# Kernel optimization log

Hardware: AMD Instinct MI355X
Metric: run time of the kernel (lower is better)

The kernel has to match this reference:

```python
import jax, jax.numpy as jnp
import numpy as np

D_MODEL = 1024
NUM_HEADS = 16
D_K = 1024
D_V = 1024
D_IN = 1024
THETA = 10000.0
B, S = 2, 2048


def setup_inputs() -> dict:
    key = jax.random.key(0)
    k1, k2, k3, k4, k5 = jax.random.split(key, 5)
    std_qkv = (2.0 / (D_IN + D_K)) ** 0.5
    std_o = (2.0 / (D_V + D_MODEL)) ** 0.5
    x = jax.random.normal(k1, (B, S, D_IN), jnp.float32)
    wq = jax.random.normal(k2, (D_IN, D_K), jnp.float32) * std_qkv
    wk = jax.random.normal(k3, (D_IN, D_K), jnp.float32) * std_qkv
    wv = jax.random.normal(k4, (D_IN, D_V), jnp.float32) * std_qkv
    wo = jax.random.normal(k5, (D_V, D_MODEL), jnp.float32) * std_o
    return {"x": x, "wq": wq, "wk": wk, "wv": wv, "wo": wo}


def _rope(t, theta):
    # t: (H, B, S, hd) -- interleaved-pair RoPE, angles pos * theta^(-2i/hd)
    hd = t.shape[-1]
    inv_freq = 1.0 / (theta ** (jnp.arange(0, hd, 2, dtype=jnp.float32) / hd))  # (hd/2,)
    pos = jnp.arange(t.shape[-2], dtype=jnp.float32)
    ang = pos[:, None] * inv_freq[None, :]                                       # (S, hd/2)
    cos, sin = jnp.cos(ang), jnp.sin(ang)
    tp = t.reshape(t.shape[:-1] + (hd // 2, 2))
    t0, t1 = tp[..., 0], tp[..., 1]
    out = jnp.stack([t0 * cos - t1 * sin, t0 * sin + t1 * cos], axis=-1)
    return out.reshape(t.shape)


def reference(x, wq, wk, wv, wo):
    b, s, _ = x.shape
    hd = D_K // NUM_HEADS
    hdv = D_V // NUM_HEADS
    # fused QKV proj (math identical to concat-then-matmul)
    q = jnp.einsum('bsd,de->bse', x, wq).reshape(b, s, NUM_HEADS, hd).transpose(2, 0, 1, 3)
    k = jnp.einsum('bsd,de->bse', x, wk).reshape(b, s, NUM_HEADS, hd).transpose(2, 0, 1, 3)
    v = jnp.einsum('bsd,de->bse', x, wv).reshape(b, s, NUM_HEADS, hdv).transpose(2, 0, 1, 3)
    q = _rope(q, THETA)
    k = _rope(k, THETA)
    scale = 1.0 / jnp.sqrt(jnp.asarray(hd, jnp.float32))
    scores = jnp.einsum('hbqd,hbkd->hbqk', q, k) * scale                 # (H,B,S,S)
    causal = jnp.tril(jnp.ones((s, s), dtype=bool))
    scores = jnp.where(causal, scores, -jnp.inf)
    attn = jax.nn.softmax(scores, axis=-1)
    o = jnp.einsum('hbqk,hbkd->hbqd', attn, v)                            # (H,B,S,hdv)
    o = o.transpose(1, 2, 0, 3).reshape(b, s, D_V)                        # merge heads (outer)
    return jnp.einsum('bsd,de->bse', o, wo)
```

## Files before the change

kernel.cpp:

```cpp
#include <hip/hip_runtime.h>
#include <stdint.h>

typedef __attribute__((ext_vector_type(8))) short short8;
typedef __attribute__((ext_vector_type(4))) float f32x4;
typedef __attribute__((ext_vector_type(4))) unsigned short ushort4v;

static __device__ __forceinline__ unsigned short f2b(float f) {
  union { float f; unsigned int u; } v; v.f = f;
  unsigned int r = v.u + 0x7FFFu + ((v.u >> 16) & 1u);
  return (unsigned short)(r >> 16);
}

static __device__ __forceinline__ float exp2fast(float x) {
#if __has_builtin(__builtin_amdgcn_exp2f)
  return __builtin_amdgcn_exp2f(x);
#else
  return exp2f(x);
#endif
}

static __device__ __forceinline__ void gload16(const void* g, void* l) {
  __builtin_amdgcn_global_load_lds(
      (const __attribute__((address_space(1))) unsigned int*)g,
      (__attribute__((address_space(3))) unsigned int*)l, 16, 0, 0);
}


__global__ __launch_bounds__(256) void cast_x_kernel(const float* __restrict__ x,
                                                     unsigned short* __restrict__ xb) {
  int i = (blockIdx.x * 256 + threadIdx.x) * 4;
  float4 v = *(const float4*)(x + i);
  ushort4v o = { f2b(v.x), f2b(v.y), f2b(v.z), f2b(v.w) };
  *(ushort4v*)(xb + i) = o;
}

__global__ __launch_bounds__(256) void transpose_cast_kernel(
    const float* __restrict__ wq, const float* __restrict__ wk,
    const float* __restrict__ wv, const float* __restrict__ wo,
    unsigned short* __restrict__ wT) {
  const int z = blockIdx.z;
  const float* src = (z == 0) ? wq : (z == 1) ? wk : (z == 2) ? wv : wo;
  unsigned short* dst = wT + (size_t)z * 1048576;
  __shared__ float t[32][33];
  const int tid = threadIdx.x;
  const int tx = tid & 31, ty = tid >> 5;
  const int n0 = blockIdx.x * 32, k0 = blockIdx.y * 32;
#pragma unroll
  for (int i = 0; i < 4; ++i) {
    int r = ty + i * 8;
    t[r][tx] = src[(size_t)(k0 + r) * 1024 + n0 + tx];
  }
  __syncthreads();
#pragma unroll
  for (int i = 0; i < 4; ++i) {
    int r = ty + i * 8;
    dst[(size_t)(n0 + r) * 1024 + k0 + tx] = f2b(t[tx][r]);
  }
}

__global__ __launch_bounds__(256) void rope_tab_kernel(float* __restrict__ ct,
                                                       float* __restrict__ st) {
  int i = blockIdx.x * 256 + threadIdx.x;
  int s = i >> 5, p = i & 31;
  float ang = (float)s * powf(10000.0f, -(float)(2 * p) / 64.0f);
  ct[i] = cosf(ang);
  st[i] = sinf(ang);
}


__global__ __launch_bounds__(256) void gemm_kernel(
    const unsigned short* __restrict__ A, const unsigned short* __restrict__ WT,
    unsigned short* __restrict__ Qb, unsigned short* __restrict__ Kb,
    unsigned short* __restrict__ VTb, float* __restrict__ Fout,
    const float* __restrict__ ctab, const float* __restrict__ stab, int finalMode) {
  __shared__ unsigned short As[128 * 32];
  __shared__ unsigned short Bs[128 * 32];
  const int tid = threadIdx.x;
  const int w = tid >> 6, lane = tid & 63;
  const int m0 = blockIdx.x * 128, n0 = blockIdx.y * 128;
  int mode;
  const unsigned short* Bt;
  if (finalMode) { mode = 3; Bt = WT; }
  else { mode = blockIdx.z; Bt = WT + (size_t)mode * 1048576; }
  const int wr = w >> 1, wc = w & 1;
  const int srow = lane >> 2, scol = lane & 3;
  f32x4 acc[4][4] = {};
  for (int k0 = 0; k0 < 1024; k0 += 32) {
#pragma unroll
    for (int c = 0; c < 2; ++c) {
      int chunk = w * 2 + c;
      gload16(A + (size_t)(m0 + chunk * 16 + srow) * 1024 + k0 + scol * 8,
              (char*)As + chunk * 1024);
      gload16(Bt + (size_t)(n0 + chunk * 16 + srow) * 1024 + k0 + scol * 8,
              (char*)Bs + chunk * 1024);
    }
    __syncthreads();
    short8 af[4], bf[4];
#pragma unroll
    for (int i = 0; i < 4; ++i) {
      af[i] = *(const short8*)((const char*)As +
              ((wr * 64 + i * 16 + (lane & 15)) * 64 + (lane >> 4) * 16));
      bf[i] = *(const short8*)((const char*)Bs +
              ((wc * 64 + i * 16 + (lane & 15)) * 64 + (lane >> 4) * 16));
    }
#pragma unroll
    for (int i = 0; i < 4; ++i)
#pragma unroll
      for (int j = 0; j < 4; ++j)
        acc[i][j] = __builtin_amdgcn_mfma_f32_16x16x32_bf16(af[i], bf[j], acc[i][j], 0, 0, 0);
    __syncthreads();
  }

  if (mode < 2) {
    unsigned short* dst = mode ? Kb : Qb;
    const float qscale = mode ? 1.0f : 0.125f * 1.44269504088896f;
#pragma unroll
    for (int i = 0; i < 4; ++i) {
#pragma unroll
      for (int j = 0; j < 4; ++j) {
        int n = n0 + wc * 64 + j * 16 + (lane & 15);
        int h = n >> 6, d = n & 63;
        int pairIdx = d >> 1;
        bool even = (n & 1) == 0;
#pragma unroll
        for (int r = 0; r < 4; ++r) {
          int m = m0 + wr * 64 + i * 16 + (lane >> 4) * 4 + r;
          int b = m >> 11, s = m & 2047;
          float v = acc[i][j][r];
          float pv = __shfl_xor(v, 1);
          float c = ctab[s * 32 + pairIdx], sn = stab[s * 32 + pairIdx];
          float ov = (even ? (v * c - pv * sn) : (pv * sn + v * c)) * qscale;
          dst[(size_t)((h * 2 + b) * 2048 + s) * 64 + d] = f2b(ov);
        }
      }
    }
  } else if (mode == 2) {
#pragma unroll
    for (int i = 0; i < 4; ++i) {
#pragma unroll
      for (int j = 0; j < 4; ++j) {
        int n = n0 + wc * 64 + j * 16 + (lane & 15);
        int h = n >> 6, d = n & 63;
        int mBase = m0 + wr * 64 + i * 16 + (lane >> 4) * 4;
        int b = mBase >> 11, s = mBase & 2047;
        ushort4v pk = { f2b(acc[i][j][0]), f2b(acc[i][j][1]),
                        f2b(acc[i][j][2]), f2b(acc[i][j][3]) };
        *(ushort4v*)(VTb + (size_t)((h * 2 + b) * 64 + d) * 2048 + s) = pk;
      }
    }
  } else {
#pragma unroll
    for (int i = 0; i < 4; ++i)
#pragma unroll
      for (int j = 0; j < 4; ++j) {
        int n = n0 + wc * 64 + j * 16 + (lane & 15);
#pragma unroll
        for (int r = 0; r < 4; ++r) {
          int m = m0 + wr * 64 + i * 16 + (lane >> 4) * 4 + r;
          Fout[(size_t)m * 1024 + n] = acc[i][j][r];
        }
      }
  }
}


__device__ __forceinline__ void proc_tile(
    const short8 aq[2], const char* Ks, const char* Vs, char* Psw,
    int lane, int w, bool diag, float* m, float* l, f32x4* o) {
  f32x4 sacc[4] = {};
  __builtin_amdgcn_s_setprio(1);
#pragma unroll
  for (int ct = 0; ct < 4; ++ct) {
    int row = ct * 16 + (lane & 15);
#pragma unroll
    for (int ks = 0; ks < 2; ++ks) {
      short8 bk = *(const short8*)(Ks + row * 128 +
                  ((ks * 64 + (lane >> 4) * 16) ^ ((row & 7) << 4)));
      sacc[ct] = __builtin_amdgcn_mfma_f32_16x16x32_bf16(aq[ks], bk, sacc[ct], 0, 0, 0);
    }
  }
  __builtin_amdgcn_s_setprio(0);
#pragma unroll
  for (int r = 0; r < 4; ++r) {
    int qrow = w * 16 + (lane >> 4) * 4 + r;
    float mx = -__builtin_inff();
#pragma unroll
    for (int ct = 0; ct < 4; ++ct) {
      float v = sacc[ct][r];
      if (diag && (ct * 16 + (lane & 15)) > qrow) v = -__builtin_inff();
      sacc[ct][r] = v;
      mx = fmaxf(mx, v);
    }
#pragma unroll
    for (int dd = 1; dd < 16; dd <<= 1) mx = fmaxf(mx, __shfl_xor(mx, dd));
    float nm = fmaxf(m[r], mx);
    float al = exp2fast(m[r] - nm);
    m[r] = nm;
    float ps = 0.f;
#pragma unroll
    for (int ct = 0; ct < 4; ++ct) {
      float pp = exp2fast(sacc[ct][r] - nm);
      sacc[ct][r] = pp;
      ps += pp;
    }
#pragma unroll
    for (int dd = 1; dd < 16; dd <<= 1) ps += __shfl_xor(ps, dd);
    l[r] = l[r] * al + ps;
#pragma unroll
    for (int ct = 0; ct < 4; ++ct) o[ct][r] *= al;
  }
#pragma unroll
  for (int ct = 0; ct < 4; ++ct)
#pragma unroll
    for (int r = 0; r < 4; ++r) {
      int row = (lane >> 4) * 4 + r;
      int cb = 2 * (ct * 16 + (lane & 15));
      *(unsigned short*)(Psw + row * 128 + (cb ^ ((row & 7) << 4))) = f2b(sacc[ct][r]);
    }
  __builtin_amdgcn_wave_barrier();
  short8 pa[2];
  {
    int row = lane & 15;
#pragma unroll
    for (int ks = 0; ks < 2; ++ks)
      pa[ks] = *(const short8*)(Psw + row * 128 +
               ((ks * 64 + (lane >> 4) * 16) ^ ((row & 7) << 4)));
  }
  __builtin_amdgcn_s_setprio(1);
#pragma unroll
  for (int ct = 0; ct < 4; ++ct) {
    int row = ct * 16 + (lane & 15);
#pragma unroll
    for (int ks = 0; ks < 2; ++ks) {
      short8 bv = *(const short8*)(Vs + row * 128 +
                  ((ks * 64 + (lane >> 4) * 16) ^ ((row & 7) << 4)));
      o[ct] = __builtin_amdgcn_mfma_f32_16x16x32_bf16(pa[ks], bv, o[ct], 0, 0, 0);
    }
  }
  __builtin_amdgcn_s_setprio(0);
}

__global__ __launch_bounds__(256) void attn_kernel(
    const unsigned short* __restrict__ Qb, const unsigned short* __restrict__ Kb,
    const unsigned short* __restrict__ VTb, unsigned short* __restrict__ Ob) {
  __shared__ unsigned short Ks[64 * 64];
  __shared__ unsigned short Vs[64 * 64];
  __shared__ unsigned short Ps[4 * 16 * 64];
  const int tid = threadIdx.x, w = tid >> 6, lane = tid & 63;
  const int p = blockIdx.x, hb = blockIdx.y;
  const int qtL = p, qtH = 31 - p;
  const int h = hb >> 1, b = hb & 1;
  const unsigned short* Qhb = Qb + (size_t)hb * 2048 * 64;
  const unsigned short* Khb = Kb + (size_t)hb * 2048 * 64;
  const unsigned short* Vhb = VTb + (size_t)hb * 64 * 2048;
  char* Psw = (char*)Ps + w * 2048;

  short8 aqL[2], aqH[2];
  {
    int rowL = qtL * 64 + w * 16 + (lane & 15);
    int rowH = qtH * 64 + w * 16 + (lane & 15);
#pragma unroll
    for (int ks = 0; ks < 2; ++ks) {
      aqL[ks] = *(const short8*)(Qhb + (size_t)rowL * 64 + ks * 32 + (lane >> 4) * 8);
      aqH[ks] = *(const short8*)(Qhb + (size_t)rowH * 64 + ks * 32 + (lane >> 4) * 8);
    }
  }
  float mL[4], lL[4], mH[4], lH[4];
#pragma unroll
  for (int r = 0; r < 4; ++r) {
    mL[r] = -__builtin_inff(); lL[r] = 0.f;
    mH[r] = -__builtin_inff(); lH[r] = 0.f;
  }
  f32x4 oL[4] = {}, oH[4] = {};

  const int r0 = tid >> 3, f0 = tid & 7;
  const int so0 = r0 * 128 + ((f0 * 16) ^ ((r0 & 7) << 4));
  short8 gK[2], gV[2];
  {
    gK[0] = *(const short8*)(Khb + (size_t)r0 * 64 + f0 * 8);
    gK[1] = *(const short8*)(Khb + (size_t)(r0 + 32) * 64 + f0 * 8);
    gV[0] = *(const short8*)(Vhb + (size_t)r0 * 2048 + f0 * 8);
    gV[1] = *(const short8*)(Vhb + (size_t)(r0 + 32) * 2048 + f0 * 8);
  }

  for (int kt = 0; kt <= qtH; ++kt) {
    *(short8*)((char*)Ks + so0) = gK[0];
    *(short8*)((char*)Ks + so0 + 32 * 128) = gK[1];
    *(short8*)((char*)Vs + so0) = gV[0];
    *(short8*)((char*)Vs + so0 + 32 * 128) = gV[1];
    __syncthreads();
    if (kt < qtH) {
      int kk0 = (kt + 1) * 64;
      gK[0] = *(const short8*)(Khb + (size_t)(kk0 + r0) * 64 + f0 * 8);
      gK[1] = *(const short8*)(Khb + (size_t)(kk0 + r0 + 32) * 64 + f0 * 8);
      gV[0] = *(const short8*)(Vhb + (size_t)r0 * 2048 + kk0 + f0 * 8);
      gV[1] = *(const short8*)(Vhb + (size_t)(r0 + 32) * 2048 + kk0 + f0 * 8);
    }
    proc_tile(aqH, (const char*)Ks, (const char*)Vs, Psw, lane, w,
              kt == qtH, mH, lH, oH);
    if (kt <= qtL)
      proc_tile(aqL, (const char*)Ks, (const char*)Vs, Psw, lane, w,
                kt == qtL, mL, lL, oL);
    __syncthreads();
  }

  float invL[4], invH[4];
#pragma unroll
  for (int r = 0; r < 4; ++r) { invL[r] = 1.0f / lL[r]; invH[r] = 1.0f / lH[r]; }
#pragma unroll
  for (int ct = 0; ct < 4; ++ct) {
    int col = h * 64 + ct * 16 + (lane & 15);
#pragma unroll
    for (int r = 0; r < 4; ++r) {
      int sL = qtL * 64 + w * 16 + (lane >> 4) * 4 + r;
      int sH = qtH * 64 + w * 16 + (lane >> 4) * 4 + r;
      Ob[(size_t)(b * 2048 + sL) * 1024 + col] = f2b(oL[ct][r] * invL[r]);
      Ob[(size_t)(b * 2048 + sH) * 1024 + col] = f2b(oH[ct][r] * invH[r]);
    }
  }
}


extern "C" void kernel_launch(void* const* d_in, const int* in_sizes, int n_in,
                              void* d_out, int out_size, void* d_ws, size_t ws_size,
                              hipStream_t stream) {
  const float* x  = (const float*)d_in[0];
  const float* wq = (const float*)d_in[1];
  const float* wk = (const float*)d_in[2];
  const float* wv = (const float*)d_in[3];
  const float* wo = (const float*)d_in[4];
  float* out = (float*)d_out;

  char* ws = (char*)d_ws;
  const size_t SZ = 8388608;
  unsigned short* xb  = (unsigned short*)(ws);
  unsigned short* wT  = (unsigned short*)(ws + SZ);
  unsigned short* Qb  = (unsigned short*)(ws + 2 * SZ);
  unsigned short* Kb  = (unsigned short*)(ws + 3 * SZ);
  unsigned short* VTb = (unsigned short*)(ws + 4 * SZ);
  unsigned short* Ob  = (unsigned short*)(ws + 5 * SZ);
  float* ctab = (float*)(ws + 6 * SZ);
  float* stab = (float*)(ws + 6 * SZ + 262144);
  if (ws_size < 6 * SZ + 2 * 262144) return;

  cast_x_kernel<<<4096, 256, 0, stream>>>(x, xb);
  transpose_cast_kernel<<<dim3(32, 32, 4), 256, 0, stream>>>(wq, wk, wv, wo, wT);
  rope_tab_kernel<<<256, 256, 0, stream>>>(ctab, stab);
  gemm_kernel<<<dim3(32, 8, 3), 256, 0, stream>>>(xb, wT, Qb, Kb, VTb, nullptr, ctab, stab, 0);
  attn_kernel<<<dim3(16, 32), 256, 0, stream>>>(Qb, Kb, VTb, Ob);
  gemm_kernel<<<dim3(32, 8, 1), 256, 0, stream>>>(Ob, wT + 3 * 1048576, Qb, Kb, VTb, out,
                                                  ctab, stab, 1);
}
```

Baseline: 151.1 us.

## Transpose attention MFMA so softmax stays in registers via bpermute, one q-tile per block

The attention kernel now computes S^T (K as the A operand, Q as B), so each lane holds one query's scores. The row max and sum then need only two cross-lane shuffles instead of four per row. P is packed to bf16 with v_cvt_pk_bf16_f32 and redistributed with ds_bpermute instead of a round trip through LDS, and the output goes through LDS for coalesced 16-byte stores. The paired low/high q-tile scheme is dropped: the grid now launches one 64-row q-tile per block, longest tiles first, and relies on the scheduler to balance the causal load.

```diff
diff --git a/kernel.cpp b/kernel.cpp
--- a/kernel.cpp
+++ b/kernel.cpp
@@ -17,6 +17,12 @@
 #else
   return exp2f(x);
 #endif
+}
+
+static __device__ __forceinline__ unsigned int cvtpk(float lo, float hi) {
+  unsigned int r;
+  asm("v_cvt_pk_bf16_f32 %0, %1, %2" : "=v"(r) : "v"(lo), "v"(hi));
+  return r;
 }
 
 static __device__ __forceinline__ void gload16(const void* g, void* l) {
@@ -164,82 +170,6 @@
 }
 
 
-__device__ __forceinline__ void proc_tile(
-    const short8 aq[2], const char* Ks, const char* Vs, char* Psw,
-    int lane, int w, bool diag, float* m, float* l, f32x4* o) {
-  f32x4 sacc[4] = {};
-  __builtin_amdgcn_s_setprio(1);
-#pragma unroll
-  for (int ct = 0; ct < 4; ++ct) {
-    int row = ct * 16 + (lane & 15);
-#pragma unroll
-    for (int ks = 0; ks < 2; ++ks) {
-      short8 bk = *(const short8*)(Ks + row * 128 +
-                  ((ks * 64 + (lane >> 4) * 16) ^ ((row & 7) << 4)));
-      sacc[ct] = __builtin_amdgcn_mfma_f32_16x16x32_bf16(aq[ks], bk, sacc[ct], 0, 0, 0);
-    }
-  }
-  __builtin_amdgcn_s_setprio(0);
-#pragma unroll
-  for (int r = 0; r < 4; ++r) {
-    int qrow = w * 16 + (lane >> 4) * 4 + r;
-    float mx = -__builtin_inff();
-#pragma unroll
-    for (int ct = 0; ct < 4; ++ct) {
-      float v = sacc[ct][r];
-      if (diag && (ct * 16 + (lane & 15)) > qrow) v = -__builtin_inff();
-      sacc[ct][r] = v;
-      mx = fmaxf(mx, v);
-    }
-#pragma unroll
-    for (int dd = 1; dd < 16; dd <<= 1) mx = fmaxf(mx, __shfl_xor(mx, dd));
-    float nm = fmaxf(m[r], mx);
-    float al = exp2fast(m[r] - nm);
-    m[r] = nm;
-    float ps = 0.f;
-#pragma unroll
-    for (int ct = 0; ct < 4; ++ct) {
-      float pp = exp2fast(sacc[ct][r] - nm);
-      sacc[ct][r] = pp;
-      ps += pp;
-    }
-#pragma unroll
-    for (int dd = 1; dd < 16; dd <<= 1) ps += __shfl_xor(ps, dd);
-    l[r] = l[r] * al + ps;
-#pragma unroll
-    for (int ct = 0; ct < 4; ++ct) o[ct][r] *= al;
-  }
-#pragma unroll
-  for (int ct = 0; ct < 4; ++ct)
-#pragma unroll
-    for (int r = 0; r < 4; ++r) {
-      int row = (lane >> 4) * 4 + r;
-      int cb = 2 * (ct * 16 + (lane & 15));
-      *(unsigned short*)(Psw + row * 128 + (cb ^ ((row & 7) << 4))) = f2b(sacc[ct][r]);
-    }
-  __builtin_amdgcn_wave_barrier();
-  short8 pa[2];
-  {
-    int row = lane & 15;
-#pragma unroll
-    for (int ks = 0; ks < 2; ++ks)
-      pa[ks] = *(const short8*)(Psw + row * 128 +
-               ((ks * 64 + (lane >> 4) * 16) ^ ((row & 7) << 4)));
-  }
-  __builtin_amdgcn_s_setprio(1);
-#pragma unroll
-  for (int ct = 0; ct < 4; ++ct) {
-    int row = ct * 16 + (lane & 15);
-#pragma unroll
-    for (int ks = 0; ks < 2; ++ks) {
-      short8 bv = *(const short8*)(Vs + row * 128 +
-                  ((ks * 64 + (lane >> 4) * 16) ^ ((row & 7) << 4)));
-      o[ct] = __builtin_amdgcn_mfma_f32_16x16x32_bf16(pa[ks], bv, o[ct], 0, 0, 0);
-    }
-  }
-  __builtin_amdgcn_s_setprio(0);
-}
-
 __global__ __launch_bounds__(256) void attn_kernel(
     const unsigned short* __restrict__ Qb, const unsigned short* __restrict__ Kb,
     const unsigned short* __restrict__ VTb, unsigned short* __restrict__ Ob) {
@@ -247,76 +177,160 @@
   __shared__ unsigned short Vs[64 * 64];
   __shared__ unsigned short Ps[4 * 16 * 64];
   const int tid = threadIdx.x, w = tid >> 6, lane = tid & 63;
-  const int p = blockIdx.x, hb = blockIdx.y;
-  const int qtL = p, qtH = 31 - p;
+  const int qt = 31 - blockIdx.x;
+  const int hb = blockIdx.y;
   const int h = hb >> 1, b = hb & 1;
+  const int qb = qt * 64;
   const unsigned short* Qhb = Qb + (size_t)hb * 2048 * 64;
   const unsigned short* Khb = Kb + (size_t)hb * 2048 * 64;
   const unsigned short* Vhb = VTb + (size_t)hb * 64 * 2048;
   char* Psw = (char*)Ps + w * 2048;
-
-  short8 aqL[2], aqH[2];
+  const int lq = lane & 15, lh = lane >> 4;
+
+  short8 aq[2];
   {
-    int rowL = qtL * 64 + w * 16 + (lane & 15);
-    int rowH = qtH * 64 + w * 16 + (lane & 15);
-#pragma unroll
-    for (int ks = 0; ks < 2; ++ks) {
-      aqL[ks] = *(const short8*)(Qhb + (size_t)rowL * 64 + ks * 32 + (lane >> 4) * 8);
-      aqH[ks] = *(const short8*)(Qhb + (size_t)rowH * 64 + ks * 32 + (lane >> 4) * 8);
-    }
-  }
-  float mL[4], lL[4], mH[4], lH[4];
-#pragma unroll
-  for (int r = 0; r < 4; ++r) {
-    mL[r] = -__builtin_inff(); lL[r] = 0.f;
-    mH[r] = -__builtin_inff(); lH[r] = 0.f;
-  }
-  f32x4 oL[4] = {}, oH[4] = {};
+    int row = qb + w * 16 + lq;
+#pragma unroll
+    for (int half = 0; half < 2; ++half)
+      aq[half] = *(const short8*)(Qhb + (size_t)row * 64 + half * 32 + lh * 8);
+  }
+  float m = -__builtin_inff(), l = 0.f;
+  f32x4 oacc[4] = {};
+  const int addrE = 4 * (lq + 32 * (lh & 1));
+  const int addrO = addrE + 64;
+  const bool lowhalf = lane < 32;
 
   const int r0 = tid >> 3, f0 = tid & 7;
   const int so0 = r0 * 128 + ((f0 * 16) ^ ((r0 & 7) << 4));
   short8 gK[2], gV[2];
-  {
-    gK[0] = *(const short8*)(Khb + (size_t)r0 * 64 + f0 * 8);
-    gK[1] = *(const short8*)(Khb + (size_t)(r0 + 32) * 64 + f0 * 8);
-    gV[0] = *(const short8*)(Vhb + (size_t)r0 * 2048 + f0 * 8);
-    gV[1] = *(const short8*)(Vhb + (size_t)(r0 + 32) * 2048 + f0 * 8);
-  }
-
-  for (int kt = 0; kt <= qtH; ++kt) {
+  gK[0] = *(const short8*)(Khb + (size_t)r0 * 64 + f0 * 8);
+  gK[1] = *(const short8*)(Khb + (size_t)(r0 + 32) * 64 + f0 * 8);
+  gV[0] = *(const short8*)(Vhb + (size_t)r0 * 2048 + f0 * 8);
+  gV[1] = *(const short8*)(Vhb + (size_t)(r0 + 32) * 2048 + f0 * 8);
+
+  for (int kt = 0; kt <= qt; ++kt) {
     *(short8*)((char*)Ks + so0) = gK[0];
     *(short8*)((char*)Ks + so0 + 32 * 128) = gK[1];
     *(short8*)((char*)Vs + so0) = gV[0];
     *(short8*)((char*)Vs + so0 + 32 * 128) = gV[1];
     __syncthreads();
-    if (kt < qtH) {
+    if (kt < qt) {
       int kk0 = (kt + 1) * 64;
       gK[0] = *(const short8*)(Khb + (size_t)(kk0 + r0) * 64 + f0 * 8);
       gK[1] = *(const short8*)(Khb + (size_t)(kk0 + r0 + 32) * 64 + f0 * 8);
       gV[0] = *(const short8*)(Vhb + (size_t)r0 * 2048 + kk0 + f0 * 8);
       gV[1] = *(const short8*)(Vhb + (size_t)(r0 + 32) * 2048 + kk0 + f0 * 8);
     }
-    proc_tile(aqH, (const char*)Ks, (const char*)Vs, Psw, lane, w,
-              kt == qtH, mH, lH, oH);
-    if (kt <= qtL)
-      proc_tile(aqL, (const char*)Ks, (const char*)Vs, Psw, lane, w,
-                kt == qtL, mL, lL, oL);
+
+    f32x4 sacc[4] = {};
+    __builtin_amdgcn_s_setprio(1);
+#pragma unroll
+    for (int ct = 0; ct < 4; ++ct) {
+      int row = ct * 16 + lq;
+#pragma unroll
+      for (int half = 0; half < 2; ++half) {
+        short8 ak = *(const short8*)((const char*)Ks + row * 128 +
+                    ((half * 64 + lh * 16) ^ ((row & 7) << 4)));
+        sacc[ct] = __builtin_amdgcn_mfma_f32_16x16x32_bf16(ak, aq[half], sacc[ct], 0, 0, 0);
+      }
+    }
+    __builtin_amdgcn_s_setprio(0);
+
+    if (kt == qt) {
+      int rel = (w * 16 + lq) - 4 * lh;
+#pragma unroll
+      for (int ct = 0; ct < 4; ++ct)
+#pragma unroll
+        for (int r = 0; r < 4; ++r)
+          if (ct * 16 + r > rel) sacc[ct][r] = -__builtin_inff();
+    }
+
+    float mx0 = fmaxf(fmaxf(sacc[0][0], sacc[0][1]), fmaxf(sacc[0][2], sacc[0][3]));
+    float mx1 = fmaxf(fmaxf(sacc[1][0], sacc[1][1]), fmaxf(sacc[1][2], sacc[1][3]));
+    float mx2 = fmaxf(fmaxf(sacc[2][0], sacc[2][1]), fmaxf(sacc[2][2], sacc[2][3]));
+    float mx3 = fmaxf(fmaxf(sacc[3][0], sacc[3][1]), fmaxf(sacc[3][2], sacc[3][3]));
+    float mx = fmaxf(fmaxf(mx0, mx1), fmaxf(mx2, mx3));
+    mx = fmaxf(mx, __shfl_xor(mx, 16));
+    mx = fmaxf(mx, __shfl_xor(mx, 32));
+    float nm = fmaxf(m, mx);
+    float al = exp2fast(m - nm);
+    m = nm;
+    float ps = 0.f;
+#pragma unroll
+    for (int ct = 0; ct < 4; ++ct)
+#pragma unroll
+      for (int r = 0; r < 4; ++r) {
+        float p = exp2fast(sacc[ct][r] - nm);
+        sacc[ct][r] = p;
+        ps += p;
+      }
+    ps += __shfl_xor(ps, 16);
+    ps += __shfl_xor(ps, 32);
+    l = l * al + ps;
+#pragma unroll
+    for (int ct = 0; ct < 4; ++ct)
+#pragma unroll
+      for (int r = 0; r < 4; ++r) oacc[ct][r] *= al;
+
+    unsigned int pkA[4], pkB[4];
+#pragma unroll
+    for (int c = 0; c < 4; ++c) {
+      pkA[c] = cvtpk(sacc[c][0], sacc[c][1]);
+      pkB[c] = cvtpk(sacc[c][2], sacc[c][3]);
+    }
+#pragma unroll
+    for (int half = 0; half < 2; ++half) {
+      int cb = half * 2;
+      union { unsigned int u[4]; short8 s; } F;
+      {
+        unsigned int t0 = __builtin_amdgcn_ds_bpermute(addrE, (int)pkA[cb]);
+        unsigned int t1 = __builtin_amdgcn_ds_bpermute(addrE, (int)pkA[cb + 1]);
+        F.u[0] = lowhalf ? t0 : t1;
+      }
+      {
+        unsigned int t0 = __builtin_amdgcn_ds_bpermute(addrE, (int)pkB[cb]);
+        unsigned int t1 = __builtin_amdgcn_ds_bpermute(addrE, (int)pkB[cb + 1]);
+        F.u[1] = lowhalf ? t0 : t1;
+      }
+      {
+        unsigned int t0 = __builtin_amdgcn_ds_bpermute(addrO, (int)pkA[cb]);
+        unsigned int t1 = __builtin_amdgcn_ds_bpermute(addrO, (int)pkA[cb + 1]);
+        F.u[2] = lowhalf ? t0 : t1;
+      }
+      {
+        unsigned int t0 = __builtin_amdgcn_ds_bpermute(addrO, (int)pkB[cb]);
+        unsigned int t1 = __builtin_amdgcn_ds_bpermute(addrO, (int)pkB[cb + 1]);
+        F.u[3] = lowhalf ? t0 : t1;
+      }
+      __builtin_amdgcn_s_setprio(1);
+#pragma unroll
+      for (int ct = 0; ct < 4; ++ct) {
+        int row = ct * 16 + lq;
+        short8 av = *(const short8*)((const char*)Vs + row * 128 +
+                    ((half * 64 + lh * 16) ^ ((row & 7) << 4)));
+        oacc[ct] = __builtin_amdgcn_mfma_f32_16x16x32_bf16(av, F.s, oacc[ct], 0, 0, 0);
+      }
+      __builtin_amdgcn_s_setprio(0);
+    }
     __syncthreads();
   }
 
-  float invL[4], invH[4];
-#pragma unroll
-  for (int r = 0; r < 4; ++r) { invL[r] = 1.0f / lL[r]; invH[r] = 1.0f / lH[r]; }
-#pragma unroll
-  for (int ct = 0; ct < 4; ++ct) {
-    int col = h * 64 + ct * 16 + (lane & 15);
+  float invl = 1.0f / l;
+#pragma unroll
+  for (int ct = 0; ct < 4; ++ct)
 #pragma unroll
     for (int r = 0; r < 4; ++r) {
-      int sL = qtL * 64 + w * 16 + (lane >> 4) * 4 + r;
-      int sH = qtH * 64 + w * 16 + (lane >> 4) * 4 + r;
-      Ob[(size_t)(b * 2048 + sL) * 1024 + col] = f2b(oL[ct][r] * invL[r]);
-      Ob[(size_t)(b * 2048 + sH) * 1024 + col] = f2b(oH[ct][r] * invH[r]);
-    }
+      int d = ct * 16 + lh * 4 + r;
+      *(unsigned short*)(Psw + lq * 128 + ((2 * d) ^ ((lq & 7) << 4))) =
+          f2b(oacc[ct][r] * invl);
+    }
+  __syncthreads();
+#pragma unroll
+  for (int pass = 0; pass < 2; ++pass) {
+    int q2 = pass * 8 + (lane >> 3), d0 = (lane & 7) * 8;
+    short8 vrow = *(const short8*)(Psw + q2 * 128 + ((2 * d0) ^ ((q2 & 7) << 4)));
+    int s = qb + w * 16 + q2;
+    *(short8*)(Ob + ((size_t)(b * 2048 + s)) * 1024 + h * 64 + d0) = vrow;
   }
 }
 
@@ -347,7 +361,7 @@
   transpose_cast_kernel<<<dim3(32, 32, 4), 256, 0, stream>>>(wq, wk, wv, wo, wT);
   rope_tab_kernel<<<256, 256, 0, stream>>>(ctab, stab);
   gemm_kernel<<<dim3(32, 8, 3), 256, 0, stream>>>(xb, wT, Qb, Kb, VTb, nullptr, ctab, stab, 0);
-  attn_kernel<<<dim3(16, 32), 256, 0, stream>>>(Qb, Kb, VTb, Ob);
+  attn_kernel<<<dim3(32, 32), 256, 0, stream>>>(Qb, Kb, VTb, Ob);
   gemm_kernel<<<dim3(32, 8, 1), 256, 0, stream>>>(Ob, wT + 3 * 1048576, Qb, Kb, VTb, out,
                                                   ctab, stab, 1);
 }
```

Result: slower. 170.3 us (+12.7%).
